# Kernel optimization log

Measured on AMD Instinct MI355X. Metric: run time of the kernel, lower is better.

The kernel has to match this reference:

```python
import jax, jax.numpy as jnp
import numpy as np

N_HOPS = 2
N_ENTITIES = 100000
EMB = 64
N_REL = 32
N_EDGES = 1000000


def _l2norm(x, eps=1e-12):
    # torch F.normalize: x / max(||x||_2, eps) per row
    n = jnp.sqrt(jnp.sum(x * x, axis=1, keepdims=True))
    return x / jnp.maximum(n, eps)


def setup_inputs() -> dict:
    key = jax.random.key(0)
    k1, k2, k3, k4, k5, k6 = jax.random.split(key, 6)
    return {
        "entity_emb": jax.random.normal(k1, (N_ENTITIES, EMB), dtype=jnp.float32),
        "edge_emb": jax.random.normal(k2, (N_REL, EMB), dtype=jnp.float32) * 0.1,
        "q_w": jax.random.normal(k3, (EMB, EMB), dtype=jnp.float32) * (1.0 / np.sqrt(EMB)),
        "k_w": jax.random.normal(k4, (EMB, EMB), dtype=jnp.float32) * (1.0 / np.sqrt(EMB)),
        "edge_index": jax.random.randint(k5, (2, N_EDGES), 0, N_ENTITIES, dtype=jnp.int32),
        "edge_type": jax.random.randint(k6, (N_EDGES,), 0, N_REL, dtype=jnp.int32),
        "mess_dropout": 0,
    }


def reference(entity_emb, edge_emb, q_w, k_w, edge_index, edge_type, mess_dropout):
    head = edge_index[0]
    tail = edge_index[1]
    rel = edge_emb[edge_type]                      # [E, D]
    kg = jnp.zeros_like(entity_emb)
    agg = entity_emb
    for _ in range(N_HOPS):
        # edge-wise tanh attention score
        left = (agg @ q_w)[head]                   # [E, D] (factor GEMM out of gather)
        right = jnp.tanh((rel * agg[tail]) @ k_w)  # [E, D]
        att = jnp.sum(left * right, axis=1)        # [E]
        # scatter_softmax over head segments
        m = jax.ops.segment_max(att, head, num_segments=N_ENTITIES)
        e = jnp.exp(att - jax.lax.stop_gradient(m)[head])
        denom = jax.ops.segment_sum(e, head, num_segments=N_ENTITIES)
        w = e / denom[head]                        # [E]
        # weighted messages + scatter_mean aggregation
        msg = w[:, None] * rel * agg[tail]         # [E, D]
        s = jax.ops.segment_sum(msg, head, num_segments=N_ENTITIES)
        cnt = jax.ops.segment_sum(jnp.ones_like(w), head, num_segments=N_ENTITIES)
        agg = s / jnp.maximum(cnt, 1.0)[:, None]
        # mess_dropout=False path; normalize + residual accumulation
        agg = _l2norm(agg)
        kg = kg + agg + entity_emb
    return kg
```

## Files before the change

### kernel.cpp

```cpp
#include <hip/hip_runtime.h>
#include <math.h>

#define EMB 64
#define MAXREL 32
#define BSHIFT 9
#define BCAP 6912
#define CH 2048

typedef short bf16x8 __attribute__((ext_vector_type(8)));
typedef float f32x4 __attribute__((ext_vector_type(4)));

__device__ __forceinline__ short f2bf(float f) {
    unsigned u = __float_as_uint(f);
    u += 0x7FFFu + ((u >> 16) & 1u);
    return (short)(u >> 16);
}

#if __has_builtin(__builtin_amdgcn_cvt_pk_bf16_f32)
__device__ __forceinline__ short2 cvt2(float a, float b) {
    return __builtin_bit_cast(short2, __builtin_amdgcn_cvt_pk_bf16_f32(a, b));
}
#else
__device__ __forceinline__ short2 cvt2(float a, float b) {
    return make_short2(f2bf(a), f2bf(b));
}
#endif

__device__ __forceinline__ float lo_bf(unsigned d) { return __uint_as_float(d << 16); }
__device__ __forceinline__ float hi_bf(unsigned d) { return __uint_as_float(d & 0xffff0000u); }
__device__ __forceinline__ float bfs(short s) {
    return __uint_as_float(((unsigned)(unsigned short)s) << 16);
}

__device__ __forceinline__ bf16x8 pack8bf(uint4 U, float4 r0, float4 r1) {
    short2 c0 = cvt2(lo_bf(U.x) * r0.x, hi_bf(U.x) * r0.y);
    short2 c1 = cvt2(lo_bf(U.y) * r0.z, hi_bf(U.y) * r0.w);
    short2 c2 = cvt2(lo_bf(U.z) * r1.x, hi_bf(U.z) * r1.y);
    short2 c3 = cvt2(lo_bf(U.w) * r1.z, hi_bf(U.w) * r1.w);
    bf16x8 a;
    a[0] = c0.x; a[1] = c0.y; a[2] = c1.x; a[3] = c1.y;
    a[4] = c2.x; a[5] = c2.y; a[6] = c3.x; a[7] = c3.y;
    return a;
}

__device__ __forceinline__ float fast_rcp(float x) {
#if __has_builtin(__builtin_amdgcn_rcpf)
    return __builtin_amdgcn_rcpf(x);
#else
    return 1.0f / x;
#endif
}

__device__ __forceinline__ float fast_tanh(float x) {
    float ax = fabsf(x);
    float z = __expf(2.0f * ax);
    float r = 1.0f - 2.0f * fast_rcp(z + 1.0f);
    return copysignf(r, x);
}

__global__ void init_kernel(short4* __restrict__ aggbf, float4* __restrict__ kg,
                            const float4* __restrict__ ent, int* __restrict__ deg,
                            int n4, int N) {
    int i = blockIdx.x * blockDim.x + threadIdx.x;
    if (i < n4) {
        float4 v = ent[i];
        short2 c0 = cvt2(v.x, v.y), c1 = cvt2(v.z, v.w);
        aggbf[i] = make_short4(c0.x, c0.y, c1.x, c1.y);
        kg[i] = make_float4(0.f, 0.f, 0.f, 0.f);
    }
    if (i < N) deg[i] = 0;
}


__global__ void hist_kernel(int* __restrict__ deg, const int* __restrict__ head, int E) {
    int e = blockIdx.x * blockDim.x + threadIdx.x;
    if (e < E) atomicAdd(&deg[head[e]], 1);
}

__global__ void scan_blocks(const int* __restrict__ deg, int* __restrict__ excl,
                            int* __restrict__ bsum, int n) {
    __shared__ int wsum[4];
    int base = blockIdx.x * 1024;
    int t = threadIdx.x;
    int lane = t & 63, wid = t >> 6;
    int idx = base + t * 4;
    int v0 = (idx + 0 < n) ? deg[idx + 0] : 0;
    int v1 = (idx + 1 < n) ? deg[idx + 1] : 0;
    int v2 = (idx + 2 < n) ? deg[idx + 2] : 0;
    int v3 = (idx + 3 < n) ? deg[idx + 3] : 0;
    int s0 = v0, s1 = s0 + v1, s2 = s1 + v2, s3 = s2 + v3;
    int tsum = s3;
    int inc = tsum;
#pragma unroll
    for (int o = 1; o < 64; o <<= 1) { int u = __shfl_up(inc, o, 64); if (lane >= o) inc += u; }
    if (lane == 63) wsum[wid] = inc;
    __syncthreads();
    int woff = 0;
#pragma unroll
    for (int w = 0; w < 4; ++w) if (w < wid) woff += wsum[w];
    int texcl = woff + inc - tsum;
    if (idx + 0 < n) excl[idx + 0] = texcl;
    if (idx + 1 < n) excl[idx + 1] = texcl + s0;
    if (idx + 2 < n) excl[idx + 2] = texcl + s1;
    if (idx + 3 < n) excl[idx + 3] = texcl + s2;
    if (t == 255) bsum[blockIdx.x] = woff + inc;
}

__global__ void scan_sums(int* __restrict__ bsum, int* __restrict__ excl, int nb, int n, int E) {
    __shared__ int ws[4];
    int t = threadIdx.x;
    if (nb > 256) {
        if (t == 0) {
            int acc = 0;
            for (int b = 0; b < nb; ++b) { int v = bsum[b]; bsum[b] = acc; acc += v; }
            excl[n] = E;
        }
        return;
    }
    int lane = t & 63, wid = t >> 6;
    int v = (t < nb) ? bsum[t] : 0;
    int inc = v;
#pragma unroll
    for (int o = 1; o < 64; o <<= 1) { int u = __shfl_up(inc, o, 64); if (lane >= o) inc += u; }
    if (lane == 63) ws[wid] = inc;
    __syncthreads();
    int woff = 0;
#pragma unroll
    for (int w = 0; w < 4; ++w) if (w < wid) woff += ws[w];
    if (t < nb) bsum[t] = woff + inc - v;
    if (t == 0) excl[n] = E;
}

__global__ void scan_add(int* __restrict__ excl, const int* __restrict__ bsum,
                         int* __restrict__ bcursor, int n) {
    int i = blockIdx.x * blockDim.x + threadIdx.x;
    if (i < n) {
        int v = excl[i] + bsum[i >> 10];
        excl[i] = v;
        if ((i & ((1 << BSHIFT) - 1)) == 0) bcursor[i >> BSHIFT] = v;
    }
}

__global__ void bucket_scatter(const int* __restrict__ head, const int* __restrict__ tail,
                               const int* __restrict__ etype, int* __restrict__ bcursor,
                               int2* __restrict__ tmp, int E, int nb) {
    __shared__ int lcnt[512];
    __shared__ int lbase[512];
    int t = threadIdx.x;
    int base = blockIdx.x * CH;
    for (int i = t; i < 512; i += 256) lcnt[i] = 0;
    __syncthreads();
    int myh[8];
#pragma unroll
    for (int i = 0; i < 8; ++i) {
        int e = base + i * 256 + t;
        if (e < E) {
            int h = head[e];
            myh[i] = h;
            atomicAdd(&lcnt[h >> BSHIFT], 1);
        } else myh[i] = -1;
    }
    __syncthreads();
    for (int b = t; b < nb; b += 256) {
        int c = lcnt[b];
        lbase[b] = (c > 0) ? atomicAdd(&bcursor[b], c) : 0;
        lcnt[b] = 0;
    }
    __syncthreads();
#pragma unroll
    for (int i = 0; i < 8; ++i) {
        int e = base + i * 256 + t;
        if (e < E) {
            int h = myh[i];
            int b = h >> BSHIFT;
            int pos = lbase[b] + atomicAdd(&lcnt[b], 1);
            tmp[pos] = make_int2(h, tail[e] | (etype[e] << 20));
        }
    }
}

__global__ void bucket_sort(const int* __restrict__ offsets, const int2* __restrict__ tmp,
                            int2* __restrict__ spair, int N) {
    __shared__ int2 staged[BCAP];
    __shared__ int lcur[1 << BSHIFT];
    int b = blockIdx.x;
    int h0 = b << BSHIFT;
    int h1 = min(h0 + (1 << BSHIFT), N);
    int r0 = offsets[h0], r1 = offsets[h1];
    int cnt = r1 - r0;
    int t = threadIdx.x;
    for (int h = h0 + t; h < h1; h += blockDim.x) lcur[h - h0] = offsets[h] - r0;
    __syncthreads();
    if (cnt <= BCAP) {
        for (int i = t; i < cnt; i += blockDim.x) {
            int2 rec = tmp[r0 + i];
            int lp = atomicAdd(&lcur[rec.x - h0], 1);
            staged[lp] = rec;
        }
        __syncthreads();
        for (int i = t; i < cnt; i += blockDim.x) spair[r0 + i] = staged[i];
    } else {
        for (int i = t; i < cnt; i += blockDim.x) {
            int2 rec = tmp[r0 + i];
            int lp = atomicAdd(&lcur[rec.x - h0], 1);
            spair[r0 + lp] = rec;
        }
    }
}


__device__ __forceinline__ void build_bfrags(bf16x8 bfrag[2][4], const float* __restrict__ W,
                                             int lane) {
    int koff = (lane >> 4) * 8;
    int n = lane & 15;
#pragma unroll
    for (int kh = 0; kh < 2; ++kh)
#pragma unroll
        for (int nt = 0; nt < 4; ++nt) {
            bf16x8 b;
#pragma unroll
            for (int j = 0; j < 8; ++j)
                b[j] = f2bf(W[(kh * 32 + koff + j) * EMB + nt * 16 + n]);
            bfrag[kh][nt] = b;
        }
}

__global__ void qproj_mfma_kernel(short* __restrict__ Qbf, const short* __restrict__ aggbf,
                                  const float* __restrict__ qw, int N) {
    int lane = threadIdx.x & 63;
    int gwave = blockIdx.x * (blockDim.x >> 6) + (threadIdx.x >> 6);
    int nwaves = gridDim.x * (blockDim.x >> 6);
    int row = lane & 15;
    int g = lane >> 4;
    int koff = g * 8;

    bf16x8 bfrag[2][4];
    build_bfrags(bfrag, qw, lane);

    int ntiles = (N + 15) >> 4;
    for (int tile = gwave; tile < ntiles; tile += nwaves) {
        int rIdx = min(tile * 16 + row, N - 1);
        const short* rowp = aggbf + (size_t)rIdx * EMB;
        bf16x8 a0 = *(const bf16x8*)(rowp + koff);
        bf16x8 a1 = *(const bf16x8*)(rowp + 32 + koff);
#pragma unroll
        for (int nt = 0; nt < 4; ++nt) {
            f32x4 acc = {0.f, 0.f, 0.f, 0.f};
            acc = __builtin_amdgcn_mfma_f32_16x16x32_bf16(a0, bfrag[0][nt], acc, 0, 0, 0);
            acc = __builtin_amdgcn_mfma_f32_16x16x32_bf16(a1, bfrag[1][nt], acc, 0, 0, 0);
#pragma unroll
            for (int reg = 0; reg < 4; ++reg) {
                int n2 = tile * 16 + g * 4 + reg;
                if (n2 < N) Qbf[(size_t)n2 * EMB + nt * 16 + (lane & 15)] = f2bf(acc[reg]);
            }
        }
    }
}

__global__ void att_mfma_kernel(float* __restrict__ att,
                                const short* __restrict__ aggbf, const short* __restrict__ Qbf,
                                const float* __restrict__ eemb, const float* __restrict__ kw,
                                const int2* __restrict__ spair, int E) {
    int lane = threadIdx.x & 63;
    int gwave = blockIdx.x * (blockDim.x >> 6) + (threadIdx.x >> 6);
    int nwaves = gridDim.x * (blockDim.x >> 6);
    int row = lane & 15;
    int g = lane >> 4;

    bf16x8 bfrag[2][4];
    build_bfrags(bfrag, kw, lane);

    int ntiles = (E + 15) >> 4;
    int tile = gwave;
    int2 pr = make_int2(0, 0);
    uint4 U0 = make_uint4(0, 0, 0, 0), U1 = make_uint4(0, 0, 0, 0);
    if (tile < ntiles) {
        pr = spair[min(tile * 16 + row, E - 1)];
        const uint4* rowa = (const uint4*)(aggbf + (size_t)(pr.y & 0xFFFFF) * EMB);
        U0 = rowa[g];
        U1 = rowa[4 + g];
    }
    for (; tile < ntiles; tile += nwaves) {
        int tnext = tile + nwaves;
        int2 prn = pr;
        if (tnext < ntiles) prn = spair[min(tnext * 16 + row, E - 1)];

        int h = pr.x;
        unsigned r = ((unsigned)pr.y) >> 20;
        const float4* rl4 = (const float4*)(eemb + (size_t)r * EMB);
        float4 y0 = rl4[g * 2], y1 = rl4[g * 2 + 1];
        float4 y2 = rl4[8 + g * 2], y3 = rl4[8 + g * 2 + 1];
        bf16x8 a0 = pack8bf(U0, y0, y1);
        bf16x8 a1 = pack8bf(U1, y2, y3);

        uint4 U0n = U0, U1n = U1;
        if (tnext < ntiles) {
            const uint4* rowan = (const uint4*)(aggbf + (size_t)(prn.y & 0xFFFFF) * EMB);
            U0n = rowan[g];
            U1n = rowan[4 + g];
        }

        int h2r0 = __shfl(h, g * 4 + 0, 64);
        int h2r1 = __shfl(h, g * 4 + 1, 64);
        int h2r2 = __shfl(h, g * 4 + 2, 64);
        int h2r3 = __shfl(h, g * 4 + 3, 64);
        const short* q0 = Qbf + (size_t)h2r0 * EMB + row;
        const short* q1 = Qbf + (size_t)h2r1 * EMB + row;
        const short* q2 = Qbf + (size_t)h2r2 * EMB + row;
        const short* q3 = Qbf + (size_t)h2r3 * EMB + row;

        float sums0 = 0.f, sums1 = 0.f, sums2 = 0.f, sums3 = 0.f;
#pragma unroll
        for (int nt = 0; nt < 4; ++nt) {
            f32x4 acc = {0.f, 0.f, 0.f, 0.f};
            acc = __builtin_amdgcn_mfma_f32_16x16x32_bf16(a0, bfrag[0][nt], acc, 0, 0, 0);
            acc = __builtin_amdgcn_mfma_f32_16x16x32_bf16(a1, bfrag[1][nt], acc, 0, 0, 0);
            sums0 += bfs(q0[nt * 16]) * fast_tanh(acc[0]);
            sums1 += bfs(q1[nt * 16]) * fast_tanh(acc[1]);
            sums2 += bfs(q2[nt * 16]) * fast_tanh(acc[2]);
            sums3 += bfs(q3[nt * 16]) * fast_tanh(acc[3]);
        }
#pragma unroll
        for (int m = 1; m <= 8; m <<= 1) {
            sums0 += __shfl_xor(sums0, m, 64);
            sums1 += __shfl_xor(sums1, m, 64);
            sums2 += __shfl_xor(sums2, m, 64);
            sums3 += __shfl_xor(sums3, m, 64);
        }
#pragma unroll
        for (int reg = 0; reg < 4; ++reg) {
            int row2 = g * 4 + reg;
            int e2 = tile * 16 + row2;
            float v = (reg == 0) ? sums0 : (reg == 1) ? sums1 : (reg == 2) ? sums2 : sums3;
            if (row == reg && e2 < E) att[e2] = v;
        }
        pr = prn; U0 = U0n; U1 = U1n;
    }
}

__global__ void head_agg_kernel(short* __restrict__ aggNewBf, float* __restrict__ kg,
                                const float* __restrict__ att, const short* __restrict__ aggOldBf,
                                const float* __restrict__ eemb, const float* __restrict__ ent,
                                const int* __restrict__ offsets, const int2* __restrict__ spair,
                                int N, int R) {
    __shared__ float4 elds4[MAXREL * 16];

    int tid = threadIdx.x;
    int lane = tid & 63;
    int wid = tid >> 6;
    int RS = (R < MAXREL) ? R : MAXREL;
    for (int i = tid; i < RS * 16; i += blockDim.x) elds4[i] = ((const float4*)eemb)[i];
    __syncthreads();

    int sub = lane >> 4;
    int q = lane & 15;
    int h = (blockIdx.x * (blockDim.x >> 6) + wid) * 4 + sub;
    if (h >= N) return;
    int beg = offsets[h], end = offsets[h + 1];
    int deg = end - beg;
    int qbase = lane & 48;

    float4 acc4 = make_float4(0.f, 0.f, 0.f, 0.f);
    float ssum = 0.f;

    auto body = [&](float ej, int trj) {
        int tj = trj & 0xFFFFF;
        unsigned rj = ((unsigned)trj) >> 20;
        float4 ew = (rj < (unsigned)RS) ? elds4[rj * 16 + q]
                                        : ((const float4*)eemb)[(size_t)rj * 16 + q];
        uint2 X = ((const uint2*)(aggOldBf + (size_t)tj * EMB))[q];
        acc4.x += ej * ew.x * lo_bf(X.x);
        acc4.y += ej * ew.y * hi_bf(X.x);
        acc4.z += ej * ew.z * lo_bf(X.y);
        acc4.w += ej * ew.w * hi_bf(X.y);
    };

    if (deg <= 16) {
        int e = beg + q;
        bool valid = q < deg;
        float av = valid ? att[e] : -3.4e38f;
        int tr = valid ? spair[e].y : 0;
        float m = av;
#pragma unroll
        for (int o = 1; o <= 8; o <<= 1) m = fmaxf(m, __shfl_xor(m, o, 64));
        float ev = valid ? __expf(av - m) : 0.f;
        ssum = ev;
        auto B = [&](int j) { body(__shfl(ev, qbase | j, 64), __shfl(tr, qbase | j, 64)); };
        int j = 0;
        for (; j + 4 <= deg; j += 4) { B(j); B(j + 1); B(j + 2); B(j + 3); }
        for (; j < deg; ++j) B(j);
    } else {
        float m = -3.4e38f;
        for (int e = beg + q; e < end; e += 16) m = fmaxf(m, att[e]);
#pragma unroll
        for (int o = 1; o <= 8; o <<= 1) m = fmaxf(m, __shfl_xor(m, o, 64));

        for (int c = beg; c < end; c += 16) {
            int e = c + q;
            float ev = 0.f; int tr = 0;
            if (e < end) {
                ev = __expf(att[e] - m);
                tr = spair[e].y;
            }
            ssum += ev;
            int nc = min(16, end - c);
            auto B = [&](int j) { body(__shfl(ev, qbase | j, 64), __shfl(tr, qbase | j, 64)); };
            if (nc == 16) {
#pragma unroll 4
                for (int j = 0; j < 16; ++j) B(j);
            } else {
                int j = 0;
                for (; j + 4 <= nc; j += 4) { B(j); B(j + 1); B(j + 2); B(j + 3); }
                for (; j < nc; ++j) B(j);
            }
        }
    }
#pragma unroll
    for (int o = 1; o <= 8; o <<= 1) ssum += __shfl_xor(ssum, o, 64);

    float scale = (deg > 0) ? 1.0f / (ssum * (float)deg) : 0.f;
    float4 v = make_float4(acc4.x * scale, acc4.y * scale, acc4.z * scale, acc4.w * scale);
    float ss = v.x * v.x + v.y * v.y + v.z * v.z + v.w * v.w;
#pragma unroll
    for (int o = 1; o <= 8; o <<= 1) ss += __shfl_xor(ss, o, 64);
    float rinv = 1.0f / fmaxf(sqrtf(ss), 1e-12f);
    v.x *= rinv; v.y *= rinv; v.z *= rinv; v.w *= rinv;

    short2 c0 = cvt2(v.x, v.y), c1 = cvt2(v.z, v.w);
    ((short4*)aggNewBf)[(size_t)h * 16 + q] = make_short4(c0.x, c0.y, c1.x, c1.y);
    float4 kgv = ((float4*)kg)[(size_t)h * 16 + q];
    float4 ev2 = ((const float4*)ent)[(size_t)h * 16 + q];
    kgv.x += v.x + ev2.x; kgv.y += v.y + ev2.y;
    kgv.z += v.z + ev2.z; kgv.w += v.w + ev2.w;
    ((float4*)kg)[(size_t)h * 16 + q] = kgv;
}

extern "C" void kernel_launch(void* const* d_in, const int* in_sizes, int n_in,
                              void* d_out, int out_size, void* d_ws, size_t ws_size,
                              hipStream_t stream) {
    const float* ent  = (const float*)d_in[0];
    const float* eemb = (const float*)d_in[1];
    const float* qw   = (const float*)d_in[2];
    const float* kw   = (const float*)d_in[3];
    const int* eidx  = (const int*)d_in[4];
    const int* etype = (const int*)d_in[5];

    const int N = in_sizes[0] / EMB;
    const int R = in_sizes[1] / EMB;
    const int E = in_sizes[5];
    const int* head = eidx;
    const int* tail = eidx + E;

    float* kg = (float*)d_out;

    float* att   = (float*)d_ws;
    int2* spair  = (int2*)(att + E);
    int* offsets = (int*)(spair + E);
    int* deg     = offsets + (N + 1);
    int* bcursor = deg + N;
    int* bsum    = bcursor + N;
    uintptr_t pa = ((uintptr_t)(bsum + 1024) + 15) & ~(uintptr_t)15;
    short* aggbf_a = (short*)pa;
    short* aggbf_b = aggbf_a + (size_t)N * EMB;
    short* Qbf     = aggbf_b + (size_t)N * EMB;
    int2* tmp      = (int2*)Qbf;

    const int NT = 256;
    const int nb = (N + 1023) / 1024;
    const int nbk = (N + (1 << BSHIFT) - 1) >> BSHIFT;

    init_kernel<<<(N * EMB / 4 + NT - 1) / NT, NT, 0, stream>>>(
        (short4*)aggbf_a, (float4*)kg, (const float4*)ent, deg, N * EMB / 4, N);
    hist_kernel<<<(E + NT - 1) / NT, NT, 0, stream>>>(deg, head, E);
    scan_blocks<<<nb, NT, 0, stream>>>(deg, offsets, bsum, N);
    scan_sums<<<1, NT, 0, stream>>>(bsum, offsets, nb, N, E);
    scan_add<<<(N + NT - 1) / NT, NT, 0, stream>>>(offsets, bsum, bcursor, N);
    bucket_scatter<<<(E + CH - 1) / CH, NT, 0, stream>>>(head, tail, etype, bcursor, tmp, E, nbk);
    bucket_sort<<<nbk, NT, 0, stream>>>(offsets, tmp, spair, N);

    short* curbf = aggbf_a;
    short* nxtbf = aggbf_b;
    for (int hop = 0; hop < 2; ++hop) {
        qproj_mfma_kernel<<<1024, NT, 0, stream>>>(Qbf, curbf, qw, N);
        att_mfma_kernel<<<2048, NT, 0, stream>>>(att, curbf, Qbf, eemb, kw, spair, E);
        head_agg_kernel<<<(N + 15) / 16, NT, 0, stream>>>(nxtbf, kg, att, curbf,
                                                          eemb, ent, offsets, spair, N, R);
        short* ts = curbf; curbf = nxtbf; nxtbf = ts;
    }
}
```

Before: 407.3 us.

## Fuse histogram into init, fold scan_sums into scan_add, simplify tanh

Merges the degree histogram into the init kernel, with deg cleared by a memset beforehand. Removes the single-block scan_sums kernel by having each scan_add block serially sum the preceding block totals itself. Rewrites fast_tanh as an exp2-based (z-1)/(z+1) form with a clamp, and hoists the kg/ent loads in head_agg ahead of the aggregation loop so their latency can overlap. The aim is fewer kernel launches and cheaper tanh, at the cost of redundant serial prefix sums per block (up to about 98 loads) and slightly different tanh numerics for large negative inputs.

```diff
diff --git a/kernel.cpp b/kernel.cpp
--- a/kernel.cpp
+++ b/kernel.cpp
@@ -52,15 +52,14 @@
 }
 
 __device__ __forceinline__ float fast_tanh(float x) {
-    float ax = fabsf(x);
-    float z = __expf(2.0f * ax);
-    float r = 1.0f - 2.0f * fast_rcp(z + 1.0f);
-    return copysignf(r, x);
+    float xa = fminf(x, 15.0f);
+    float z = exp2f(2.885390082f * xa);
+    return (z - 1.0f) * fast_rcp(z + 1.0f);
 }
 
 __global__ void init_kernel(short4* __restrict__ aggbf, float4* __restrict__ kg,
                             const float4* __restrict__ ent, int* __restrict__ deg,
-                            int n4, int N) {
+                            const int* __restrict__ head, int n4, int E) {
     int i = blockIdx.x * blockDim.x + threadIdx.x;
     if (i < n4) {
         float4 v = ent[i];
@@ -68,14 +67,9 @@
         aggbf[i] = make_short4(c0.x, c0.y, c1.x, c1.y);
         kg[i] = make_float4(0.f, 0.f, 0.f, 0.f);
     }
-    if (i < N) deg[i] = 0;
-}
-
-
-__global__ void hist_kernel(int* __restrict__ deg, const int* __restrict__ head, int E) {
-    int e = blockIdx.x * blockDim.x + threadIdx.x;
-    if (e < E) atomicAdd(&deg[head[e]], 1);
-}
+    if (i < E) atomicAdd(&deg[head[i]], 1);
+}
+
 
 __global__ void scan_blocks(const int* __restrict__ deg, int* __restrict__ excl,
                             int* __restrict__ bsum, int n) {
@@ -106,39 +100,24 @@
     if (t == 255) bsum[blockIdx.x] = woff + inc;
 }
 
-__global__ void scan_sums(int* __restrict__ bsum, int* __restrict__ excl, int nb, int n, int E) {
-    __shared__ int ws[4];
-    int t = threadIdx.x;
-    if (nb > 256) {
-        if (t == 0) {
-            int acc = 0;
-            for (int b = 0; b < nb; ++b) { int v = bsum[b]; bsum[b] = acc; acc += v; }
-            excl[n] = E;
-        }
-        return;
-    }
-    int lane = t & 63, wid = t >> 6;
-    int v = (t < nb) ? bsum[t] : 0;
-    int inc = v;
-#pragma unroll
-    for (int o = 1; o < 64; o <<= 1) { int u = __shfl_up(inc, o, 64); if (lane >= o) inc += u; }
-    if (lane == 63) ws[wid] = inc;
-    __syncthreads();
-    int woff = 0;
-#pragma unroll
-    for (int w = 0; w < 4; ++w) if (w < wid) woff += ws[w];
-    if (t < nb) bsum[t] = woff + inc - v;
-    if (t == 0) excl[n] = E;
-}
-
 __global__ void scan_add(int* __restrict__ excl, const int* __restrict__ bsum,
-                         int* __restrict__ bcursor, int n) {
-    int i = blockIdx.x * blockDim.x + threadIdx.x;
+                         int* __restrict__ bcursor, int n, int E) {
+    __shared__ int pref0;
+    int blockBase = blockIdx.x * blockDim.x;
+    int b0 = blockBase >> 10;
+    if (threadIdx.x == 0) {
+        int acc = 0;
+        for (int j = 0; j < b0; ++j) acc += bsum[j];
+        pref0 = acc;
+    }
+    __syncthreads();
+    int i = blockBase + threadIdx.x;
     if (i < n) {
-        int v = excl[i] + bsum[i >> 10];
+        int v = excl[i] + pref0;
         excl[i] = v;
         if ((i & ((1 << BSHIFT) - 1)) == 0) bcursor[i >> BSHIFT] = v;
     }
+    if (blockIdx.x == 0 && threadIdx.x == 0) excl[n] = E;
 }
 
 __global__ void bucket_scatter(const int* __restrict__ head, const int* __restrict__ tail,
@@ -359,6 +338,9 @@
     int beg = offsets[h], end = offsets[h + 1];
     int deg = end - beg;
     int qbase = lane & 48;
+
+    float4 kgv = ((float4*)kg)[(size_t)h * 16 + q];
+    float4 ev2 = ((const float4*)ent)[(size_t)h * 16 + q];
 
     float4 acc4 = make_float4(0.f, 0.f, 0.f, 0.f);
     float ssum = 0.f;
@@ -428,8 +410,6 @@
 
     short2 c0 = cvt2(v.x, v.y), c1 = cvt2(v.z, v.w);
     ((short4*)aggNewBf)[(size_t)h * 16 + q] = make_short4(c0.x, c0.y, c1.x, c1.y);
-    float4 kgv = ((float4*)kg)[(size_t)h * 16 + q];
-    float4 ev2 = ((const float4*)ent)[(size_t)h * 16 + q];
     kgv.x += v.x + ev2.x; kgv.y += v.y + ev2.y;
     kgv.z += v.z + ev2.z; kgv.w += v.w + ev2.w;
     ((float4*)kg)[(size_t)h * 16 + q] = kgv;
@@ -469,12 +449,11 @@
     const int nb = (N + 1023) / 1024;
     const int nbk = (N + (1 << BSHIFT) - 1) >> BSHIFT;
 
+    hipMemsetAsync(deg, 0, (size_t)N * 4, stream);
     init_kernel<<<(N * EMB / 4 + NT - 1) / NT, NT, 0, stream>>>(
-        (short4*)aggbf_a, (float4*)kg, (const float4*)ent, deg, N * EMB / 4, N);
-    hist_kernel<<<(E + NT - 1) / NT, NT, 0, stream>>>(deg, head, E);
+        (short4*)aggbf_a, (float4*)kg, (const float4*)ent, deg, head, N * EMB / 4, E);
     scan_blocks<<<nb, NT, 0, stream>>>(deg, offsets, bsum, N);
-    scan_sums<<<1, NT, 0, stream>>>(bsum, offsets, nb, N, E);
-    scan_add<<<(N + NT - 1) / NT, NT, 0, stream>>>(offsets, bsum, bcursor, N);
+    scan_add<<<(N + NT - 1) / NT, NT, 0, stream>>>(offsets, bsum, bcursor, N, E);
     bucket_scatter<<<(E + CH - 1) / CH, NT, 0, stream>>>(head, tail, etype, bcursor, tmp, E, nbk);
     bucket_sort<<<nbk, NT, 0, stream>>>(offsets, tmp, spair, N);
 
```

Measured after the change: 425.6 us. 1.05x slower.
